# Kernel optimization log

Measured on AMD Instinct MI355X. Metric: run time of the kernel, lower is better.

The kernel has to match this reference:

```python
import jax, jax.numpy as jnp
import numpy as np

N = 100000      # total nodes = B_GRAPHS * NODES_PER_GRAPH
NPG = 1000      # nodes per graph (num_nodes in module)
B_GRAPHS = 100
H = 128         # hidden_channels
CIN = 3         # in_channels
E = 1600000     # edges (avg_degree 16)
OUT = 2         # out_channels


def setup_inputs() -> dict:
    key = jax.random.key(0)
    ks = jax.random.split(key, 20)
    s = 0.05
    inp = {
        "x": jax.random.normal(ks[0], (N, CIN), jnp.float32),
        "edge_index": jnp.stack([
            jax.random.randint(ks[1], (E,), 0, N),
            jax.random.randint(ks[2], (E,), 0, N),
        ]).astype(jnp.int64),
        "batch": jnp.repeat(jnp.arange(B_GRAPHS), NPG).astype(jnp.int64),
        # DiffusionConv layer 0: CIN -> H ; layer 1: H -> H
        "W_self0": jax.random.normal(ks[3], (CIN, H), jnp.float32) * s,
        "W_nbr0": jax.random.normal(ks[4], (CIN, H), jnp.float32) * s,
        "b0": jnp.zeros((H,), jnp.float32),
        "W_self1": jax.random.normal(ks[5], (H, H), jnp.float32) * s,
        "W_nbr1": jax.random.normal(ks[6], (H, H), jnp.float32) * s,
        "b1": jnp.zeros((H,), jnp.float32),
        # 2 stacked LSTMs (torch layout: W_ih [4H, in], W_hh [4H, H])
        "Wih0": jax.random.normal(ks[7], (4 * H, H), jnp.float32) * s,
        "Whh0": jax.random.normal(ks[8], (4 * H, H), jnp.float32) * s,
        "bih0": jnp.zeros((4 * H,), jnp.float32),
        "bhh0": jnp.zeros((4 * H,), jnp.float32),
        "Wih1": jax.random.normal(ks[9], (4 * H, H), jnp.float32) * s,
        "Whh1": jax.random.normal(ks[10], (4 * H, H), jnp.float32) * s,
        "bih1": jnp.zeros((4 * H,), jnp.float32),
        "bhh1": jnp.zeros((4 * H,), jnp.float32),
        # output head
        "W_out": jax.random.normal(ks[11], (H, OUT), jnp.float32) * s,
        "b_out": jnp.zeros((OUT,), jnp.float32),
    }
    return inp


def diffusion_conv(h, src, dst, W_self, W_nbr, b):
    # gather-aggregate-transform: out = h W_self + (D^-1 A h) W_nbr + b
    msgs = h[src]                                            # [E, C] gather
    agg = jax.ops.segment_sum(msgs, dst, num_segments=N)     # [N, C] scatter-add
    deg = jax.ops.segment_sum(jnp.ones((src.shape[0], 1), h.dtype), dst,
                              num_segments=N)                # [N, 1]
    agg = agg / jnp.maximum(deg, 1.0)
    return h @ W_self + agg @ W_nbr + b


def lstm_layer(x_seq, Wih, Whh, bih, bhh):
    # x_seq: [T, Bn, H] seq-first, zero initial state (torch default)
    Bn = x_seq.shape[1]
    h0 = jnp.zeros((Bn, H), x_seq.dtype)
    c0 = jnp.zeros((Bn, H), x_seq.dtype)

    def step(carry, xt):
        h, c = carry
        g = xt @ Wih.T + h @ Whh.T + (bih + bhh)   # [Bn, 4H]
        i, f, gg, o = jnp.split(g, 4, axis=-1)     # torch gate order i,f,g,o
        c = jax.nn.sigmoid(f) * c + jax.nn.sigmoid(i) * jnp.tanh(gg)
        h = jax.nn.sigmoid(o) * jnp.tanh(c)
        return (h, c), h

    _, hs = jax.lax.scan(step, (h0, c0), x_seq)
    return hs


def reference(x, edge_index, batch, W_self0, W_nbr0, b0, W_self1, W_nbr1, b1,
              Wih0, Whh0, bih0, bhh0, Wih1, Whh1, bih1, bhh1, W_out, b_out):
    src, dst = edge_index[0], edge_index[1]
    h = jax.nn.relu(diffusion_conv(x, src, dst, W_self0, W_nbr0, b0))
    h = jax.nn.relu(diffusion_conv(h, src, dst, W_self1, W_nbr1, b1))
    # view(-1, num_nodes, hidden): [B_GRAPHS, NPG, H], LSTM seq-first
    seq = h.reshape(B_GRAPHS, NPG, H)
    seq = lstm_layer(seq, Wih0, Whh0, bih0, bhh0)
    seq = lstm_layer(seq, Wih1, Whh1, bih1, bhh1)
    h = seq.reshape(N, H)
    # global_mean_pool over batch vector
    pooled = jax.ops.segment_sum(h, batch, num_segments=B_GRAPHS)
    cnt = jax.ops.segment_sum(jnp.ones((N, 1), h.dtype), batch,
                              num_segments=B_GRAPHS)
    pooled = pooled / jnp.maximum(cnt, 1.0)
    logits = pooled @ W_out + b_out                # [B_GRAPHS, OUT]
    return jax.nn.log_softmax(logits, axis=1)
```

## Files before the change

kernel.cpp:

```cpp
#include <hip/hip_runtime.h>

#define N_NODES 100000
#define NPG     1000
#define B_GR    100
#define HDIM    128
#define E_EDGES 1600000

typedef __attribute__((ext_vector_type(8))) short bf16x8;
typedef __attribute__((ext_vector_type(4))) float f32x4;
typedef unsigned long long u64;

__device__ __forceinline__ float sigf(float x) { return 1.f / (1.f + __expf(-x)); }
__device__ __forceinline__ float tanh_fast(float x) { return 1.f - 2.f / (__expf(2.f * x) + 1.f); }
__device__ __forceinline__ unsigned short f2bf(float f) {
    unsigned u = __float_as_uint(f);
    unsigned r = (u + 0x7fffu + ((u >> 16) & 1u)) >> 16;
    return (unsigned short)r;
}

__global__ void k_count(const int* __restrict__ dst, int* __restrict__ cnt) {
    int e = blockIdx.x * 256 + threadIdx.x;
    if (e < E_EDGES) atomicAdd(&cnt[dst[e]], 1);
}

__global__ void k_scan1(const int* __restrict__ cnt, int* __restrict__ row_ptr, int* __restrict__ bsum) {
    __shared__ int sd[256];
    int tid = threadIdx.x;
    int base = blockIdx.x * 1024 + tid * 4;
    int v[4];
#pragma unroll
    for (int j = 0; j < 4; ++j) {
        int i = base + j;
        v[j] = (i < N_NODES) ? cnt[i] : 0;
    }
    int s = v[0] + v[1] + v[2] + v[3];
    sd[tid] = s;
    __syncthreads();
    for (int off = 1; off < 256; off <<= 1) {
        int t = (tid >= off) ? sd[tid - off] : 0;
        __syncthreads();
        sd[tid] += t;
        __syncthreads();
    }
    int excl = sd[tid] - s;
    int run = excl;
#pragma unroll
    for (int j = 0; j < 4; ++j) {
        int i = base + j;
        run += v[j];
        if (i < N_NODES) row_ptr[1 + i] = run;
    }
    if (tid == 255) bsum[blockIdx.x] = sd[255];
}

__global__ void k_scan2(int* __restrict__ bsum, int nb) {
    if (threadIdx.x == 0 && blockIdx.x == 0) {
        int carry = 0;
        for (int b = 0; b < nb; ++b) {
            int t = bsum[b];
            bsum[b] = carry;
            carry += t;
        }
    }
}

__global__ void k_scan3(int* __restrict__ row_ptr, const int* __restrict__ bsum, int* __restrict__ cursor) {
    int i = blockIdx.x * 256 + threadIdx.x;
    if (i >= N_NODES) return;
    int incl = row_ptr[1 + i] + bsum[i >> 10];
    row_ptr[1 + i] = incl;
    if (i == 0) { row_ptr[0] = 0; cursor[0] = 0; }
    if (i + 1 < N_NODES) cursor[i + 1] = incl;
}

__global__ void k_fill(const int* __restrict__ src, const int* __restrict__ dst,
                       int* __restrict__ cursor, int* __restrict__ csr_src) {
    int e = blockIdx.x * 256 + threadIdx.x;
    if (e >= E_EDGES) return;
    int d = dst[e];
    int pos = atomicAdd(&cursor[d], 1);
    csr_src[pos] = src[e];
}

__global__ void k_conv0(const float* __restrict__ x, const int* __restrict__ rp, const int* __restrict__ csr,
                        const float* __restrict__ Ws, const float* __restrict__ Wn, const float* __restrict__ b,
                        float* __restrict__ out) {
    int n = blockIdx.x;
    int tid = threadIdx.x;
    __shared__ float sagg[3];
    if (tid < 3) sagg[tid] = 0.f;
    __syncthreads();
    int s0 = rp[n], s1 = rp[n + 1];
    int deg = s1 - s0;
    for (int j = tid; j < deg; j += 128) {
        int s = csr[s0 + j];
        atomicAdd(&sagg[0], x[s * 3 + 0]);
        atomicAdd(&sagg[1], x[s * 3 + 1]);
        atomicAdd(&sagg[2], x[s * 3 + 2]);
    }
    __syncthreads();
    float inv = 1.f / fmaxf((float)deg, 1.f);
    float a0 = sagg[0] * inv, a1 = sagg[1] * inv, a2 = sagg[2] * inv;
    float x0 = x[n * 3 + 0], x1 = x[n * 3 + 1], x2 = x[n * 3 + 2];
    float acc = b[tid]
        + x0 * Ws[0 * 128 + tid] + x1 * Ws[1 * 128 + tid] + x2 * Ws[2 * 128 + tid]
        + a0 * Wn[0 * 128 + tid] + a1 * Wn[1 * 128 + tid] + a2 * Wn[2 * 128 + tid];
    out[n * 128 + tid] = fmaxf(acc, 0.f);
}

__global__ void k_agg(const float* __restrict__ hin, const int* __restrict__ rp, const int* __restrict__ csr,
                      float* __restrict__ out) {
    int n = blockIdx.x;
    int tid = threadIdx.x;
    __shared__ int sidx[128];
    int s0 = rp[n], s1 = rp[n + 1];
    int deg = s1 - s0;
    float acc = 0.f;
    for (int base = 0; base < deg; base += 128) {
        int m = min(128, deg - base);
        if (tid < m) sidx[tid] = csr[s0 + base + tid];
        __syncthreads();
        for (int j = 0; j < m; ++j) acc += hin[sidx[j] * 128 + tid];
        __syncthreads();
    }
    out[n * 128 + tid] = acc / fmaxf((float)deg, 1.f);
}

__global__ __launch_bounds__(256)
void k_conv1mm(const float* __restrict__ A, float* __restrict__ B,
               const float* __restrict__ Wself, const float* __restrict__ Wnbr,
               const float* __restrict__ bias) {
    __shared__ float As[64 * 64];
    __shared__ float Wls[64 * 128];
    int tid = threadIdx.x;
    int r0 = blockIdx.x * 64;
    int tx = tid & 31, ty = tid >> 5;
    float acc[8][4];
#pragma unroll
    for (int r = 0; r < 8; ++r)
#pragma unroll
        for (int j = 0; j < 4; ++j) acc[r][j] = 0.f;

    for (int chunk = 0; chunk < 4; ++chunk) {
        const float* Asrc = (chunk < 2) ? A : B;
        const float* Wsrc = (chunk < 2) ? Wself : Wnbr;
        int k0 = (chunk & 1) * 64;
#pragma unroll
        for (int i = 0; i < 4; ++i) {
            int e = tid + 256 * i;
            int row = e >> 4, c4 = e & 15;
            int grow = r0 + row;
            float4 v = make_float4(0.f, 0.f, 0.f, 0.f);
            if (grow < N_NODES) v = *(const float4*)&Asrc[grow * 128 + k0 + c4 * 4];
            *(float4*)&As[row * 64 + c4 * 4] = v;
        }
#pragma unroll
        for (int i = 0; i < 8; ++i) {
            int e = tid + 256 * i;
            int row = e >> 5, c4 = e & 31;
            *(float4*)&Wls[row * 128 + c4 * 4] = *(const float4*)&Wsrc[(k0 + row) * 128 + c4 * 4];
        }
        __syncthreads();
#pragma unroll 4
        for (int kk = 0; kk < 64; ++kk) {
            float4 w = *(const float4*)&Wls[kk * 128 + tx * 4];
#pragma unroll
            for (int r = 0; r < 8; ++r) {
                float a = As[(ty + 8 * r) * 64 + kk];
                acc[r][0] += a * w.x; acc[r][1] += a * w.y;
                acc[r][2] += a * w.z; acc[r][3] += a * w.w;
            }
        }
        __syncthreads();
    }
    float4 bb = *(const float4*)&bias[tx * 4];
#pragma unroll
    for (int r = 0; r < 8; ++r) {
        int grow = r0 + ty + 8 * r;
        if (grow < N_NODES) {
            float4 v;
            v.x = fmaxf(acc[r][0] + bb.x, 0.f);
            v.y = fmaxf(acc[r][1] + bb.y, 0.f);
            v.z = fmaxf(acc[r][2] + bb.z, 0.f);
            v.w = fmaxf(acc[r][3] + bb.w, 0.f);
            *(float4*)&B[grow * 128 + tx * 4] = v;
        }
    }
}

__global__ void k_prepf(const float* __restrict__ Wih0, const float* __restrict__ Whh0,
                        const float* __restrict__ Wih1, const float* __restrict__ Whh1,
                        unsigned short* __restrict__ WTf) {
    int idx = blockIdx.x * 256 + threadIdx.x;
    int lane = idx & 63;
    int gt = (idx >> 6) & 3;
    int kt = (idx >> 8) & 7;
    int w  = (idx >> 11) & 7;
    int l  = idx >> 14;
    int d = 16 * w + (lane & 15);
    int k0 = kt * 32 + (lane >> 4) * 8;
    int wrow = gt * 128 + d;
    const float* Wi = l ? Wih1 : Wih0;
    const float* Wh = l ? Whh1 : Whh0;
    const float* srcp = (k0 < 128) ? (Wi + wrow * 128 + k0) : (Wh + wrow * 128 + (k0 - 128));
    unsigned short o[8];
#pragma unroll
    for (int j = 0; j < 8; ++j) o[j] = f2bf(srcp[j]);
    u64 lo = (u64)o[0] | ((u64)o[1] << 16) | ((u64)o[2] << 32) | ((u64)o[3] << 48);
    u64 hi = (u64)o[4] | ((u64)o[5] << 16) | ((u64)o[6] << 32) | ((u64)o[7] << 48);
    u64* dst = (u64*)(WTf + (size_t)idx * 8);
    dst[0] = lo; dst[1] = hi;
}

__global__ void k_bsum(const float* __restrict__ bih0, const float* __restrict__ bhh0,
                       const float* __restrict__ bih1, const float* __restrict__ bhh1,
                       float* __restrict__ bs) {
    int i = blockIdx.x * 256 + threadIdx.x;
    int l = i >> 9, c = i & 511;
    bs[i] = l ? (bih1[c] + bhh1[c]) : (bih0[c] + bhh0[c]);
}

__global__ __launch_bounds__(512, 2)
void k_lstm_layer(const float* __restrict__ X32,
                  const unsigned short* __restrict__ Xf,
                  const unsigned short* __restrict__ WTf,
                  const float* __restrict__ bsL,
                  unsigned short* __restrict__ Hf_out,
                  float* __restrict__ pooled,
                  int mode) {
    __shared__ __align__(16) unsigned short xs[2048];
    __shared__ __align__(16) unsigned short hs[2048];
    int tid = threadIdx.x;
    int l = tid & 63;
    int w = tid >> 6;
    int rb = blockIdx.x;
    int n0 = rb * 16;
    int nreal = (n0 + 16 <= NPG) ? 16 : (NPG - n0);

    bf16x8 Bw[8][4];
    const bf16x8* Wv = (const bf16x8*)WTf;
#pragma unroll
    for (int kt = 0; kt < 8; ++kt)
#pragma unroll
        for (int gt = 0; gt < 4; ++gt)
            Bw[kt][gt] = Wv[((w * 8 + kt) * 4 + gt) * 64 + l];

    int d = (w << 4) | (l & 15);
    float bi = bsL[d], bf_ = bsL[128 + d], bg = bsL[256 + d], bo = bsL[384 + d];
    float cst0 = 0.f, cst1 = 0.f, cst2 = 0.f, cst3 = 0.f;

    int ktp = d >> 5, oct = (d >> 3) & 3, boff = d & 7;
    int hbase = ktp * 512 + ((l >> 4) * 4 + 16 * oct) * 8 + boff;

    ((u64*)hs)[tid] = 0ull;
    __syncthreads();

    for (int t = 0; t < 100; ++t) {
        if (mode == 0) {
            int r = tid & 15, g = tid >> 4;
            int row = n0 + r;
            f32x4 v = {0.f, 0.f, 0.f, 0.f};
            if (row < NPG) v = *(const f32x4*)(X32 + (size_t)(t * NPG + row) * 128 + g * 4);
            unsigned short h0 = f2bf(v.x), h1 = f2bf(v.y), h2 = f2bf(v.z), h3 = f2bf(v.w);
            u64 pk = (u64)h0 | ((u64)h1 << 16) | ((u64)h2 << 32) | ((u64)h3 << 48);
            int dd = g * 4;
            int hw = (dd >> 5) * 512 + (r + 16 * ((dd >> 3) & 3)) * 8 + (dd & 7);
            *(u64*)(xs + hw) = pk;
        } else {
            const u64* srcp = (const u64*)(Xf + (size_t)(t * 63 + rb) * 2048);
            ((u64*)xs)[tid] = srcp[tid];
        }
        __syncthreads();

        f32x4 acc[4];
#pragma unroll
        for (int gt = 0; gt < 4; ++gt) acc[gt] = (f32x4){0.f, 0.f, 0.f, 0.f};
#pragma unroll
        for (int kt = 0; kt < 8; ++kt) {
            const unsigned short* base = (kt < 4) ? xs : hs;
            bf16x8 a = *(const bf16x8*)(base + (kt & 3) * 512 + l * 8);
            acc[0] = __builtin_amdgcn_mfma_f32_16x16x32_bf16(a, Bw[kt][0], acc[0], 0, 0, 0);
            acc[1] = __builtin_amdgcn_mfma_f32_16x16x32_bf16(a, Bw[kt][1], acc[1], 0, 0, 0);
            acc[2] = __builtin_amdgcn_mfma_f32_16x16x32_bf16(a, Bw[kt][2], acc[2], 0, 0, 0);
            acc[3] = __builtin_amdgcn_mfma_f32_16x16x32_bf16(a, Bw[kt][3], acc[3], 0, 0, 0);
        }
        __syncthreads();

        float hsum = 0.f;
#pragma unroll
        for (int reg = 0; reg < 4; ++reg) {
            float gi = acc[0][reg] + bi;
            float gf = acc[1][reg] + bf_;
            float gg = acc[2][reg] + bg;
            float go = acc[3][reg] + bo;
            float cprev = (reg == 0) ? cst0 : (reg == 1) ? cst1 : (reg == 2) ? cst2 : cst3;
            float c = sigf(gf) * cprev + sigf(gi) * tanh_fast(gg);
            if (reg == 0) cst0 = c; else if (reg == 1) cst1 = c; else if (reg == 2) cst2 = c; else cst3 = c;
            float h = sigf(go) * tanh_fast(c);
            unsigned short hb = f2bf(h);
            hs[hbase + reg * 8] = hb;
            if (mode == 0) {
                Hf_out[(size_t)(t * 63 + rb) * 2048 + hbase + reg * 8] = hb;
            } else {
                int row = (l >> 4) * 4 + reg;
                if (row < nreal) hsum += h;
            }
        }
        if (mode == 1) {
            hsum += __shfl_xor(hsum, 16);
            hsum += __shfl_xor(hsum, 32);
            if ((l >> 4) == 0) atomicAdd(&pooled[t * 128 + d], hsum);
        }
        __syncthreads();
    }
}

__global__ void k_head(const float* __restrict__ pooled, const float* __restrict__ Wout,
                       const float* __restrict__ bout, float* __restrict__ out) {
    int gi = threadIdx.x;
    if (gi >= B_GR) return;
    float l0 = bout[0], l1 = bout[1];
    for (int d = 0; d < 128; ++d) {
        float p = pooled[gi * 128 + d] / 1000.0f;
        l0 += p * Wout[d * 2 + 0];
        l1 += p * Wout[d * 2 + 1];
    }
    float m = fmaxf(l0, l1);
    float lse = m + logf(__expf(l0 - m) + __expf(l1 - m));
    out[gi * 2 + 0] = l0 - lse;
    out[gi * 2 + 1] = l1 - lse;
}

extern "C" void kernel_launch(void* const* d_in, const int* in_sizes, int n_in,
                              void* d_out, int out_size, void* d_ws, size_t ws_size,
                              hipStream_t stream) {
    const float* x    = (const float*)d_in[0];
    const int*   ei   = (const int*)d_in[1];
    const int*   srcI = ei;
    const int*   dstI = ei + E_EDGES;
    const float* Ws0  = (const float*)d_in[3];
    const float* Wn0  = (const float*)d_in[4];
    const float* b0   = (const float*)d_in[5];
    const float* Ws1  = (const float*)d_in[6];
    const float* Wn1  = (const float*)d_in[7];
    const float* b1   = (const float*)d_in[8];
    const float* Wih0 = (const float*)d_in[9];
    const float* Whh0 = (const float*)d_in[10];
    const float* bih0 = (const float*)d_in[11];
    const float* bhh0 = (const float*)d_in[12];
    const float* Wih1 = (const float*)d_in[13];
    const float* Whh1 = (const float*)d_in[14];
    const float* bih1 = (const float*)d_in[15];
    const float* bhh1 = (const float*)d_in[16];
    const float* Wout = (const float*)d_in[17];
    const float* bout = (const float*)d_in[18];
    float* out = (float*)d_out;

    char* ws = (char*)d_ws;
    int*   row_ptr = (int*)(ws + 0);
    int*   cursor  = (int*)(ws + 400128);
    int*   csr_src = (int*)(ws + 800128);
    int*   bsum    = (int*)(ws + 7200128);
    float* bufA    = (float*)(ws + 7200640);
    float* bufB    = (float*)(ws + 58400640);
    unsigned short* WTf = (unsigned short*)(ws + 109600640);
    float* bsB     = (float*)(ws + 110649216);
    float* pooled  = (float*)(ws + 110653312);

    unsigned short* H0f = (unsigned short*)bufA;

    hipMemsetAsync(cursor, 0, N_NODES * sizeof(int), stream);
    hipMemsetAsync(pooled, 0, B_GR * 128 * sizeof(float), stream);

    k_count<<<E_EDGES / 256, 256, 0, stream>>>(dstI, cursor);
    k_scan1<<<98, 256, 0, stream>>>(cursor, row_ptr, bsum);
    k_scan2<<<1, 64, 0, stream>>>(bsum, 98);
    k_scan3<<<(N_NODES + 255) / 256, 256, 0, stream>>>(row_ptr, bsum, cursor);
    k_fill<<<E_EDGES / 256, 256, 0, stream>>>(srcI, dstI, cursor, csr_src);

    k_conv0<<<N_NODES, 128, 0, stream>>>(x, row_ptr, csr_src, Ws0, Wn0, b0, bufA);
    k_agg<<<N_NODES, 128, 0, stream>>>(bufA, row_ptr, csr_src, bufB);
    k_conv1mm<<<(N_NODES + 63) / 64, 256, 0, stream>>>(bufA, bufB, Ws1, Wn1, b1);

    k_prepf<<<128, 256, 0, stream>>>(Wih0, Whh0, Wih1, Whh1, WTf);
    k_bsum<<<4, 256, 0, stream>>>(bih0, bhh0, bih1, bhh1, bsB);

    k_lstm_layer<<<63, 512, 0, stream>>>(bufB, nullptr, WTf, bsB, H0f, nullptr, 0);
    k_lstm_layer<<<63, 512, 0, stream>>>(nullptr, H0f, WTf + 131072, bsB + 512, nullptr, pooled, 1);

    k_head<<<1, 128, 0, stream>>>(pooled, Wout, bout, out);
}
```

Before: 1.007 ms.

## Register-prefetch LSTM inputs, double-buffer hidden state, cut per-step barriers

The LSTM recurrence kernel now loads each timestep's input directly into registers in MFMA fragment layout and prefetches the next step's input during the current step, instead of staging it through shared memory. The hidden state is double-buffered in LDS, which removes two of the three per-step barriers. Layer-0 hidden outputs are written with coalesced 64-bit stores from the shared buffer one step late, replacing scattered 16-bit global stores. This shortens the serial per-timestep critical path, at the cost of more registers and dropping the 2-blocks-per-CU launch bound.

```diff
diff --git a/kernel.cpp b/kernel.cpp
--- a/kernel.cpp
+++ b/kernel.cpp
@@ -9,13 +9,22 @@
 typedef __attribute__((ext_vector_type(8))) short bf16x8;
 typedef __attribute__((ext_vector_type(4))) float f32x4;
 typedef unsigned long long u64;
+typedef unsigned short u16;
 
 __device__ __forceinline__ float sigf(float x) { return 1.f / (1.f + __expf(-x)); }
 __device__ __forceinline__ float tanh_fast(float x) { return 1.f - 2.f / (__expf(2.f * x) + 1.f); }
-__device__ __forceinline__ unsigned short f2bf(float f) {
+__device__ __forceinline__ u16 f2bf(float f) {
     unsigned u = __float_as_uint(f);
     unsigned r = (u + 0x7fffu + ((u >> 16) & 1u)) >> 16;
-    return (unsigned short)r;
+    return (u16)r;
+}
+__device__ __forceinline__ bf16x8 pack8(f32x4 a, f32x4 b) {
+    bf16x8 r;
+    r[0] = (short)f2bf(a[0]); r[1] = (short)f2bf(a[1]);
+    r[2] = (short)f2bf(a[2]); r[3] = (short)f2bf(a[3]);
+    r[4] = (short)f2bf(b[0]); r[5] = (short)f2bf(b[1]);
+    r[6] = (short)f2bf(b[2]); r[7] = (short)f2bf(b[3]);
+    return r;
 }
 
 __global__ void k_count(const int* __restrict__ dst, int* __restrict__ cnt) {
@@ -190,7 +199,7 @@
 
 __global__ void k_prepf(const float* __restrict__ Wih0, const float* __restrict__ Whh0,
                         const float* __restrict__ Wih1, const float* __restrict__ Whh1,
-                        unsigned short* __restrict__ WTf) {
+                        u16* __restrict__ WTf) {
     int idx = blockIdx.x * 256 + threadIdx.x;
     int lane = idx & 63;
     int gt = (idx >> 6) & 3;
@@ -203,13 +212,12 @@
     const float* Wi = l ? Wih1 : Wih0;
     const float* Wh = l ? Whh1 : Whh0;
     const float* srcp = (k0 < 128) ? (Wi + wrow * 128 + k0) : (Wh + wrow * 128 + (k0 - 128));
-    unsigned short o[8];
+    u16 o[8];
 #pragma unroll
     for (int j = 0; j < 8; ++j) o[j] = f2bf(srcp[j]);
-    u64 lo = (u64)o[0] | ((u64)o[1] << 16) | ((u64)o[2] << 32) | ((u64)o[3] << 48);
-    u64 hi = (u64)o[4] | ((u64)o[5] << 16) | ((u64)o[6] << 32) | ((u64)o[7] << 48);
     u64* dst = (u64*)(WTf + (size_t)idx * 8);
-    dst[0] = lo; dst[1] = hi;
+    dst[0] = (u64)o[0] | ((u64)o[1] << 16) | ((u64)o[2] << 32) | ((u64)o[3] << 48);
+    dst[1] = (u64)o[4] | ((u64)o[5] << 16) | ((u64)o[6] << 32) | ((u64)o[7] << 48);
 }
 
 __global__ void k_bsum(const float* __restrict__ bih0, const float* __restrict__ bhh0,
@@ -220,25 +228,20 @@
     bs[i] = l ? (bih1[c] + bhh1[c]) : (bih0[c] + bhh0[c]);
 }
 
-__global__ __launch_bounds__(512, 2)
-void k_lstm_layer(const float* __restrict__ X32,
-                  const unsigned short* __restrict__ Xf,
-                  const unsigned short* __restrict__ WTf,
-                  const float* __restrict__ bsL,
-                  unsigned short* __restrict__ Hf_out,
-                  float* __restrict__ pooled,
-                  int mode) {
-    __shared__ __align__(16) unsigned short xs[2048];
-    __shared__ __align__(16) unsigned short hs[2048];
+__global__ __launch_bounds__(512)
+void k_lstm_layer(const float* __restrict__ X32, const u16* __restrict__ Xf,
+                  const u16* __restrict__ WTl, const float* __restrict__ bsL,
+                  u16* __restrict__ H0f, float* __restrict__ pooled, int mode) {
+    __shared__ __align__(16) u16 hsh[2][2048];
     int tid = threadIdx.x;
     int l = tid & 63;
     int w = tid >> 6;
     int rb = blockIdx.x;
     int n0 = rb * 16;
-    int nreal = (n0 + 16 <= NPG) ? 16 : (NPG - n0);
+    int nreal = min(16, NPG - n0);
 
     bf16x8 Bw[8][4];
-    const bf16x8* Wv = (const bf16x8*)WTf;
+    const bf16x8* Wv = (const bf16x8*)WTl;
 #pragma unroll
     for (int kt = 0; kt < 8; ++kt)
 #pragma unroll
@@ -252,39 +255,78 @@
     int ktp = d >> 5, oct = (d >> 3) & 3, boff = d & 7;
     int hbase = ktp * 512 + ((l >> 4) * 4 + 16 * oct) * 8 + boff;
 
-    ((u64*)hs)[tid] = 0ull;
+    int rowq = min(n0 + (l & 15), NPG - 1);
+    int koff = (l >> 4) * 8;
+    const float* x32p = X32 ? (X32 + (size_t)rowq * 128 + koff) : nullptr;
+    const u16*  xfp  = Xf ? (Xf + (size_t)rb * 2048 + l * 8) : nullptr;
+
+    f32x4 xr[8];
+    bf16x8 xf[4];
+    if (mode == 0) {
+#pragma unroll
+        for (int kt = 0; kt < 4; ++kt) {
+            xr[2 * kt]     = *(const f32x4*)(x32p + kt * 32);
+            xr[2 * kt + 1] = *(const f32x4*)(x32p + kt * 32 + 4);
+        }
+    } else {
+#pragma unroll
+        for (int kt = 0; kt < 4; ++kt)
+            xf[kt] = *(const bf16x8*)(xfp + kt * 512);
+    }
+
+    ((u64*)hsh[0])[tid] = 0ull;
     __syncthreads();
+    int cur = 0;
 
     for (int t = 0; t < 100; ++t) {
+        bf16x8 xa[4];
         if (mode == 0) {
-            int r = tid & 15, g = tid >> 4;
-            int row = n0 + r;
-            f32x4 v = {0.f, 0.f, 0.f, 0.f};
-            if (row < NPG) v = *(const f32x4*)(X32 + (size_t)(t * NPG + row) * 128 + g * 4);
-            unsigned short h0 = f2bf(v.x), h1 = f2bf(v.y), h2 = f2bf(v.z), h3 = f2bf(v.w);
-            u64 pk = (u64)h0 | ((u64)h1 << 16) | ((u64)h2 << 32) | ((u64)h3 << 48);
-            int dd = g * 4;
-            int hw = (dd >> 5) * 512 + (r + 16 * ((dd >> 3) & 3)) * 8 + (dd & 7);
-            *(u64*)(xs + hw) = pk;
+#pragma unroll
+            for (int kt = 0; kt < 4; ++kt) xa[kt] = pack8(xr[2 * kt], xr[2 * kt + 1]);
         } else {
-            const u64* srcp = (const u64*)(Xf + (size_t)(t * 63 + rb) * 2048);
-            ((u64*)xs)[tid] = srcp[tid];
-        }
-        __syncthreads();
+#pragma unroll
+            for (int kt = 0; kt < 4; ++kt) xa[kt] = xf[kt];
+        }
 
         f32x4 acc[4];
 #pragma unroll
         for (int gt = 0; gt < 4; ++gt) acc[gt] = (f32x4){0.f, 0.f, 0.f, 0.f};
 #pragma unroll
-        for (int kt = 0; kt < 8; ++kt) {
-            const unsigned short* base = (kt < 4) ? xs : hs;
-            bf16x8 a = *(const bf16x8*)(base + (kt & 3) * 512 + l * 8);
-            acc[0] = __builtin_amdgcn_mfma_f32_16x16x32_bf16(a, Bw[kt][0], acc[0], 0, 0, 0);
-            acc[1] = __builtin_amdgcn_mfma_f32_16x16x32_bf16(a, Bw[kt][1], acc[1], 0, 0, 0);
-            acc[2] = __builtin_amdgcn_mfma_f32_16x16x32_bf16(a, Bw[kt][2], acc[2], 0, 0, 0);
-            acc[3] = __builtin_amdgcn_mfma_f32_16x16x32_bf16(a, Bw[kt][3], acc[3], 0, 0, 0);
-        }
-        __syncthreads();
+        for (int kt = 0; kt < 4; ++kt) {
+            acc[0] = __builtin_amdgcn_mfma_f32_16x16x32_bf16(xa[kt], Bw[kt][0], acc[0], 0, 0, 0);
+            acc[1] = __builtin_amdgcn_mfma_f32_16x16x32_bf16(xa[kt], Bw[kt][1], acc[1], 0, 0, 0);
+            acc[2] = __builtin_amdgcn_mfma_f32_16x16x32_bf16(xa[kt], Bw[kt][2], acc[2], 0, 0, 0);
+            acc[3] = __builtin_amdgcn_mfma_f32_16x16x32_bf16(xa[kt], Bw[kt][3], acc[3], 0, 0, 0);
+        }
+        __syncthreads();
+
+        if (mode == 0 && t > 0)
+            ((u64*)(H0f + (size_t)((t - 1) * 63 + rb) * 2048))[tid] = ((const u64*)hsh[cur])[tid];
+
+        if (t < 99) {
+            if (mode == 0) {
+                const float* xn = x32p + (size_t)(t + 1) * NPG * 128;
+#pragma unroll
+                for (int kt = 0; kt < 4; ++kt) {
+                    xr[2 * kt]     = *(const f32x4*)(xn + kt * 32);
+                    xr[2 * kt + 1] = *(const f32x4*)(xn + kt * 32 + 4);
+                }
+            } else {
+                const u16* xn = xfp + (size_t)(t + 1) * 63 * 2048;
+#pragma unroll
+                for (int kt = 0; kt < 4; ++kt)
+                    xf[kt] = *(const bf16x8*)(xn + kt * 512);
+            }
+        }
+
+#pragma unroll
+        for (int kt = 4; kt < 8; ++kt) {
+            bf16x8 af = *(const bf16x8*)(hsh[cur] + (kt & 3) * 512 + l * 8);
+            acc[0] = __builtin_amdgcn_mfma_f32_16x16x32_bf16(af, Bw[kt][0], acc[0], 0, 0, 0);
+            acc[1] = __builtin_amdgcn_mfma_f32_16x16x32_bf16(af, Bw[kt][1], acc[1], 0, 0, 0);
+            acc[2] = __builtin_amdgcn_mfma_f32_16x16x32_bf16(af, Bw[kt][2], acc[2], 0, 0, 0);
+            acc[3] = __builtin_amdgcn_mfma_f32_16x16x32_bf16(af, Bw[kt][3], acc[3], 0, 0, 0);
+        }
 
         float hsum = 0.f;
 #pragma unroll
@@ -297,11 +339,8 @@
             float c = sigf(gf) * cprev + sigf(gi) * tanh_fast(gg);
             if (reg == 0) cst0 = c; else if (reg == 1) cst1 = c; else if (reg == 2) cst2 = c; else cst3 = c;
             float h = sigf(go) * tanh_fast(c);
-            unsigned short hb = f2bf(h);
-            hs[hbase + reg * 8] = hb;
-            if (mode == 0) {
-                Hf_out[(size_t)(t * 63 + rb) * 2048 + hbase + reg * 8] = hb;
-            } else {
+            hsh[cur ^ 1][hbase + reg * 8] = f2bf(h);
+            if (mode == 1) {
                 int row = (l >> 4) * 4 + reg;
                 if (row < nreal) hsum += h;
             }
@@ -311,7 +350,11 @@
             hsum += __shfl_xor(hsum, 32);
             if ((l >> 4) == 0) atomicAdd(&pooled[t * 128 + d], hsum);
         }
-        __syncthreads();
+        cur ^= 1;
+    }
+    if (mode == 0) {
+        __syncthreads();
+        ((u64*)(H0f + (size_t)(99 * 63 + rb) * 2048))[tid] = ((const u64*)hsh[cur])[tid];
     }
 }
 
@@ -363,11 +406,11 @@
     int*   bsum    = (int*)(ws + 7200128);
     float* bufA    = (float*)(ws + 7200640);
     float* bufB    = (float*)(ws + 58400640);
-    unsigned short* WTf = (unsigned short*)(ws + 109600640);
+    u16*   WTf     = (u16*)(ws + 109600640);
     float* bsB     = (float*)(ws + 110649216);
     float* pooled  = (float*)(ws + 110653312);
 
-    unsigned short* H0f = (unsigned short*)bufA;
+    u16* H0f = (u16*)bufA;
 
     hipMemsetAsync(cursor, 0, N_NODES * sizeof(int), stream);
     hipMemsetAsync(pooled, 0, B_GR * 128 * sizeof(float), stream);
```

Result: faster. 975.9 us (-3.1%).
